# Kernel tuning notes

Hardware: AMD Instinct MI355X
Metric: run time of the kernel (lower is better)

Reference implementation:

```python
import jax, jax.numpy as jnp
import numpy as np

T, B, DIM, N = 2, 256, 512, 196


def setup_inputs() -> dict:
    key = jax.random.key(0)
    ks = jax.random.split(key, 6)
    scale_mem = (2.0 / (DIM + DIM)) ** 0.5      # GlorotNormal
    scale_cat = (2.0 / (2 * DIM + DIM)) ** 0.5
    scale_attn = (2.0 / (DIM + 1)) ** 0.5
    return {
        "memory": jax.random.normal(ks[0], (T, B, DIM), dtype=jnp.float32),
        "know": jax.random.normal(ks[1], (B, DIM, N), dtype=jnp.float32),
        "control": jax.random.normal(ks[2], (T, B, DIM), dtype=jnp.float32),
        "W_mem": jax.random.normal(ks[3], (DIM, DIM), dtype=jnp.float32) * scale_mem,
        "b_mem": jnp.zeros((DIM,), dtype=jnp.float32),
        "W_concat": jax.random.normal(ks[4], (2 * DIM, DIM), dtype=jnp.float32) * scale_cat,
        "b_concat": jnp.zeros((DIM,), dtype=jnp.float32),
        "W_attn": jax.random.normal(ks[5], (DIM, 1), dtype=jnp.float32) * scale_attn,
        "b_attn": jnp.zeros((1,), dtype=jnp.float32),
    }


def reference(memory, know, control, W_mem, b_mem, W_concat, b_concat, W_attn, b_attn):
    # mem = Dense(dim)(memory[-1]) -> [B, dim]
    mem = memory[-1] @ W_mem + b_mem
    # mem[..., None] * know -> [B, dim, N]; concat along channel axis -> [B, 2*dim, N]
    cat = jnp.concatenate([mem[:, :, None] * know, know], axis=1)
    # transpose to [B, N, 2*dim], Dense(dim) -> [B, N, dim]
    concat = jnp.swapaxes(cat, 1, 2) @ W_concat + b_concat
    # gate by control[-1] -> [B, N, dim]; Dense(1) + squeeze -> [B, N]
    attn = concat * control[-1][:, None, :]
    logits = jnp.squeeze(attn @ W_attn, -1) + b_attn[0]
    # softmax over N, then (faithfully) weighted sum over the dim axis -> [B, N]
    a = jax.nn.softmax(logits, axis=1)[:, None, :]  # [B, 1, N]
    read = jnp.sum(a * know, axis=1)  # [B, N]
    return read
```

## Files before the change

kernel.cpp:

```cpp
#include <hip/hip_runtime.h>
#include <cfloat>

#define BB   256
#define DIM  512
#define NN   196

typedef __attribute__((ext_vector_type(8))) short bf16x8;
typedef __attribute__((ext_vector_type(4))) float f32x4;

__device__ __forceinline__ ushort f2bf(float x) {
    unsigned u = __float_as_uint(x);
    return (ushort)((u + 0x7FFFu + ((u >> 16) & 1u)) >> 16);
}

__global__ __launch_bounds__(256) void convert_kernel(
    const float* __restrict__ memory, const float* __restrict__ control,
    const float* __restrict__ W_mem, const float* __restrict__ W_concat,
    const float* __restrict__ W_attn,
    ushort* __restrict__ Wt,
    ushort* __restrict__ mu)
{
    const int tid = threadIdx.x;
    const int blk = blockIdx.x;

    if (blk < 128) {
        const float4* in4 = (const float4*)W_concat;
        uint2* out = (uint2*)(Wt + (size_t)DIM * DIM);
        #pragma unroll
        for (int p = 0; p < 4; ++p) {
            const int idx = blk * 1024 + p * 256 + tid;
            const float4 q = in4[idx];
            uint2 o;
            o.x = (unsigned)f2bf(q.x) | ((unsigned)f2bf(q.y) << 16);
            o.y = (unsigned)f2bf(q.z) | ((unsigned)f2bf(q.w) << 16);
            out[idx] = o;
        }
    } else if (blk < 192) {
        __shared__ float T[64][65];
        const int t  = blk - 128;
        const int tk = (t >> 3) * 64, ti = (t & 7) * 64;
        const int r  = tid >> 2;
        const int cb = (tid & 3) * 16;
        #pragma unroll
        for (int j = 0; j < 16; j += 4) {
            const float4 q = *(const float4*)&W_mem[(size_t)(tk + r) * DIM + ti + cb + j];
            T[r][cb + j + 0] = q.x; T[r][cb + j + 1] = q.y;
            T[r][cb + j + 2] = q.z; T[r][cb + j + 3] = q.w;
        }
        __syncthreads();
        const int ii = tid & 63;
        const int kq = tid >> 6;
        #pragma unroll
        for (int kk = 0; kk < 16; kk += 2) {
            const int k = kq * 16 + kk;
            const unsigned v = (unsigned)f2bf(T[k][ii]) | ((unsigned)f2bf(T[k + 1][ii]) << 16);
            *(unsigned*)&Wt[(size_t)(ti + ii) * DIM + tk + k] = v;
        }
    } else {
        const float4* mem4 = (const float4*)(memory  + (size_t)BB * DIM);
        const float4* ctl4 = (const float4*)(control + (size_t)BB * DIM);
        const float4* wa4  = (const float4*)W_attn;
        uint2* out = (uint2*)mu;
        #pragma unroll
        for (int p = 0; p < 4; ++p) {
            const int idx = (blk - 192) * 1024 + p * 256 + tid;
            const int sec = idx >> 15;
            const int j   = idx & 32767;
            float4 q = sec ? ctl4[j] : mem4[j];
            if (sec) {
                const float4 wa = wa4[j & 127];
                q.x *= wa.x; q.y *= wa.y; q.z *= wa.z; q.w *= wa.w;
            }
            uint2 o;
            o.x = (unsigned)f2bf(q.x) | ((unsigned)f2bf(q.y) << 16);
            o.y = (unsigned)f2bf(q.z) | ((unsigned)f2bf(q.w) << 16);
            out[(size_t)sec * 32768 + j] = o;
        }
    }
}

__global__ __launch_bounds__(128) void prep_mfma(
    const ushort* __restrict__ Wt,
    const ushort* __restrict__ mu,
    const float* __restrict__ b_mem,
    float* __restrict__ w_out)
{
    __shared__ __align__(16) ushort mus[2][16][520];

    const int tid = threadIdx.x;
    const int wv  = tid >> 6;
    const int l   = tid & 63;
    const int b0  = blockIdx.x * 16;
    const int i0  = blockIdx.y * 32;

    #pragma unroll
    for (int p = 0; p < 16; ++p) {
        const int idx = p * 128 + tid;
        const int a   = idx >> 10;
        const int rb  = (idx >> 6) & 15;
        const int kc  = (idx & 63) * 8;
        *(uint4*)&mus[a][rb][kc] =
            *(const uint4*)&mu[((size_t)a * BB + b0 + rb) * DIM + kc];
    }
    __syncthreads();

    const int fr = l & 15;
    const int fk = (l >> 4) * 8;

    f32x4 accM = {0.f, 0.f, 0.f, 0.f};
    f32x4 acc1 = {0.f, 0.f, 0.f, 0.f};
    f32x4 acc2 = {0.f, 0.f, 0.f, 0.f};

    const int ib = i0 + wv * 16 + fr;
    const ushort* wm = Wt + ((size_t)0 * DIM + ib) * DIM;
    const ushort* c1 = Wt + ((size_t)1 * DIM + ib) * DIM;
    const ushort* c2 = Wt + ((size_t)2 * DIM + ib) * DIM;

    #pragma unroll 4
    for (int t = 0; t < 16; ++t) {
        const int k = t * 32 + fk;
        const bf16x8 am = *(const bf16x8*)&mus[0][fr][k];
        const bf16x8 au = *(const bf16x8*)&mus[1][fr][k];
        const bf16x8 bm = *(const bf16x8*)&wm[k];
        const bf16x8 b1 = *(const bf16x8*)&c1[k];
        const bf16x8 b2 = *(const bf16x8*)&c2[k];
        accM = __builtin_amdgcn_mfma_f32_16x16x32_bf16(am, bm, accM, 0, 0, 0);
        acc1 = __builtin_amdgcn_mfma_f32_16x16x32_bf16(au, b1, acc1, 0, 0, 0);
        acc2 = __builtin_amdgcn_mfma_f32_16x16x32_bf16(au, b2, acc2, 0, 0, 0);
    }

    const float bmv = b_mem[ib];
    const int rb0 = (l >> 4) * 4;
    #pragma unroll
    for (int r = 0; r < 4; ++r) {
        w_out[(size_t)(b0 + rb0 + r) * DIM + ib] =
            (accM[r] + bmv) * acc1[r] + acc2[r];
    }
}

__global__ __launch_bounds__(512, 4) void prep_fallback(
    const float* __restrict__ memory, const float* __restrict__ control,
    const float* __restrict__ W_mem, const float* __restrict__ b_mem,
    const float* __restrict__ W_concat, const float* __restrict__ W_attn,
    float* __restrict__ w_out)
{
    __shared__ float4 MU4[4][DIM];
    __shared__ float  buf[12288];

    const int tid = threadIdx.x;
    const int il  = tid & 31;
    const int kg  = tid >> 5;
    const int b0  = blockIdx.x * 8;
    const int i0  = blockIdx.y * 32;

    const float* mem_in = memory  + (size_t)BB * DIM;
    const float* ctl_in = control + (size_t)BB * DIM;

    {
        const float wa = W_attn[tid];
        #pragma unroll
        for (int p = 0; p < 4; ++p) {
            MU4[p][tid] = make_float4(
                mem_in[(size_t)(b0 + 2 * p)     * DIM + tid],
                ctl_in[(size_t)(b0 + 2 * p)     * DIM + tid] * wa,
                mem_in[(size_t)(b0 + 2 * p + 1) * DIM + tid],
                ctl_in[(size_t)(b0 + 2 * p + 1) * DIM + tid] * wa);
        }
    }

    float am[8] = {}, a1[8] = {}, a2[8] = {};
    const int sr = tid >> 4;
    const int sc = tid & 15;
    float2* WT = (float2*)buf;

    float4 f1 = *(const float4*)&W_concat[(size_t)(i0 + sr) * DIM + sc * 4];
    float4 f2 = *(const float4*)&W_concat[(size_t)(DIM + i0 + sr) * DIM + sc * 4];
    float wmc[4], wmn[4];
    #pragma unroll
    for (int j = 0; j < 4; ++j)
        wmc[j] = W_mem[(size_t)(kg * 4 + j) * DIM + i0 + il];

    for (int kt = 0; kt < DIM; kt += 64) {
        __syncthreads();
        {
            const float* f1f = (const float*)&f1;
            const float* f2f = (const float*)&f2;
            #pragma unroll
            for (int j = 0; j < 4; ++j)
                WT[(sc * 4 + j) * 33 + sr] = make_float2(f1f[j], f2f[j]);
        }
        if (kt + 64 < DIM) {
            f1 = *(const float4*)&W_concat[(size_t)(i0 + sr) * DIM + kt + 64 + sc * 4];
            f2 = *(const float4*)&W_concat[(size_t)(DIM + i0 + sr) * DIM + kt + 64 + sc * 4];
        }
        __syncthreads();
        if (kt + 64 < DIM) {
            #pragma unroll
            for (int j = 0; j < 4; ++j)
                wmn[j] = W_mem[(size_t)(kt + 64 + kg * 4 + j) * DIM + i0 + il];
        }
        #pragma unroll
        for (int j = 0; j < 4; ++j) {
            const int kl = kg * 4 + j;
            const int k  = kt + kl;
            const float2 c = WT[kl * 33 + il];
            #pragma unroll
            for (int p = 0; p < 4; ++p) {
                const float4 muv = MU4[p][k];
                am[2*p]   = fmaf(muv.x, wmc[j], am[2*p]);
                a1[2*p]   = fmaf(muv.y, c.x,    a1[2*p]);
                a2[2*p]   = fmaf(muv.y, c.y,    a2[2*p]);
                am[2*p+1] = fmaf(muv.z, wmc[j], am[2*p+1]);
                a1[2*p+1] = fmaf(muv.w, c.x,    a1[2*p+1]);
                a2[2*p+1] = fmaf(muv.w, c.y,    a2[2*p+1]);
            }
        }
        #pragma unroll
        for (int j = 0; j < 4; ++j) wmc[j] = wmn[j];
    }

    __syncthreads();
    #pragma unroll
    for (int b = 0; b < 8; ++b) {
        const int row = (kg * 8 + b) * 32 + il;
        buf[row]        = am[b];
        buf[4096 + row] = a1[b];
        buf[8192 + row] = a2[b];
    }
    __syncthreads();
    if (tid < 256) {
        const int rb = tid >> 5, ri = tid & 31;
        float sm = 0.f, s1 = 0.f, s2 = 0.f;
        #pragma unroll
        for (int t = 0; t < 16; ++t) {
            const int row = (t * 8 + rb) * 32 + ri;
            sm += buf[row];
            s1 += buf[4096 + row];
            s2 += buf[8192 + row];
        }
        w_out[(size_t)(b0 + rb) * DIM + i0 + ri] =
            (sm + b_mem[i0 + ri]) * s1 + s2;
    }
}

__global__ __launch_bounds__(1024) void read_kernel(
    const float* __restrict__ know,
    const float* __restrict__ w,
    float* __restrict__ out)
{
    __shared__ float  w_s[DIM];
    __shared__ float4 part_lg[16][50];
    __shared__ float4 part_ks[16][50];
    __shared__ float  tmp[256];
    __shared__ float  bc[2];

    const int tx  = threadIdx.x;
    const int ty  = threadIdx.y;
    const int tid = ty * 64 + tx;
    const int b   = blockIdx.x;

    if (tid < DIM) w_s[tid] = w[(size_t)b * DIM + tid];
    __syncthreads();

    float4 lg = make_float4(0.f, 0.f, 0.f, 0.f);
    float4 ks = make_float4(0.f, 0.f, 0.f, 0.f);
    if (tx < 49) {
        const float4* kp = (const float4*)(know + (size_t)b * DIM * NN) + (size_t)(ty * 32) * 49 + tx;
        const float*  wp = w_s + ty * 32;
        #pragma unroll 8
        for (int dd = 0; dd < 32; ++dd) {
            const float4 kv = kp[(size_t)dd * 49];
            const float  wv = wp[dd];
            lg.x = fmaf(kv.x, wv, lg.x); lg.y = fmaf(kv.y, wv, lg.y);
            lg.z = fmaf(kv.z, wv, lg.z); lg.w = fmaf(kv.w, wv, lg.w);
            ks.x += kv.x; ks.y += kv.y; ks.z += kv.z; ks.w += kv.w;
        }
        part_lg[ty][tx] = lg;
        part_ks[ty][tx] = ks;
    }
    __syncthreads();

    float lgn = 0.f, ksn = 0.f;
    if (tid < NN) {
        const int ng = tid >> 2, j = tid & 3;
        #pragma unroll
        for (int t = 0; t < 16; ++t) {
            lgn += ((const float*)&part_lg[t][ng])[j];
            ksn += ((const float*)&part_ks[t][ng])[j];
        }
    }

    if (tid < 256) tmp[tid] = (tid < NN) ? lgn : -FLT_MAX;
    __syncthreads();
    if (tid < 64) {
        float m = fmaxf(fmaxf(tmp[tid], tmp[tid + 64]),
                        fmaxf(tmp[tid + 128], tmp[tid + 192]));
        #pragma unroll
        for (int o = 32; o; o >>= 1) m = fmaxf(m, __shfl_down(m, o));
        if (tid == 0) bc[0] = m;
    }
    __syncthreads();

    const float e = (tid < NN) ? __expf(lgn - bc[0]) : 0.f;
    if (tid < 256) tmp[tid] = e;
    __syncthreads();
    if (tid < 64) {
        float s = tmp[tid] + tmp[tid + 64] + tmp[tid + 128] + tmp[tid + 192];
        #pragma unroll
        for (int o = 32; o; o >>= 1) s += __shfl_down(s, o);
        if (tid == 0) bc[1] = s;
    }
    __syncthreads();

    if (tid < NN) out[(size_t)b * NN + tid] = e / bc[1] * ksn;
}

extern "C" void kernel_launch(void* const* d_in, const int* in_sizes, int n_in,
                              void* d_out, int out_size, void* d_ws, size_t ws_size,
                              hipStream_t stream) {
    const float* memory   = (const float*)d_in[0];
    const float* know     = (const float*)d_in[1];
    const float* control  = (const float*)d_in[2];
    const float* W_mem    = (const float*)d_in[3];
    const float* b_mem    = (const float*)d_in[4];
    const float* W_concat = (const float*)d_in[5];
    const float* W_attn   = (const float*)d_in[7];
    float* outp = (float*)d_out;

    const size_t W_BYTES  = (size_t)BB * DIM * sizeof(float);
    const size_t WT_BYTES = (size_t)3 * DIM * DIM * sizeof(ushort);
    const size_t MU_BYTES = (size_t)2 * BB * DIM * sizeof(ushort);

    float* w_ws = (float*)d_ws;

    if (ws_size >= W_BYTES + WT_BYTES + MU_BYTES) {
        ushort* Wt = (ushort*)((char*)d_ws + W_BYTES);
        ushort* mu = (ushort*)((char*)d_ws + W_BYTES + WT_BYTES);
        convert_kernel<<<dim3(256), dim3(256), 0, stream>>>(
            memory, control, W_mem, W_concat, W_attn, Wt, mu);
        prep_mfma<<<dim3(BB / 16, DIM / 32), dim3(128), 0, stream>>>(
            Wt, mu, b_mem, w_ws);
    } else {
        prep_fallback<<<dim3(BB / 8, DIM / 32), dim3(512), 0, stream>>>(
            memory, control, W_mem, b_mem, W_concat, W_attn, w_ws);
    }
    read_kernel<<<dim3(BB), dim3(64, 16), 0, stream>>>(know, w_ws, outp);
}
```

Before: 33.12 us.

## Split-K the MFMA prep GEMM with atomics and defer combine to read kernel

Result: slower. 36.97 us (+11.6%).

```diff
diff --git a/kernel.cpp b/kernel.cpp
--- a/kernel.cpp
+++ b/kernel.cpp
@@ -23,21 +23,16 @@
     const int tid = threadIdx.x;
     const int blk = blockIdx.x;
 
-    if (blk < 128) {
-        const float4* in4 = (const float4*)W_concat;
-        uint2* out = (uint2*)(Wt + (size_t)DIM * DIM);
-        #pragma unroll
-        for (int p = 0; p < 4; ++p) {
-            const int idx = blk * 1024 + p * 256 + tid;
-            const float4 q = in4[idx];
-            uint2 o;
-            o.x = (unsigned)f2bf(q.x) | ((unsigned)f2bf(q.y) << 16);
-            o.y = (unsigned)f2bf(q.z) | ((unsigned)f2bf(q.w) << 16);
-            out[idx] = o;
-        }
-    } else if (blk < 192) {
+    if (blk < 512) {
+        const int idx = blk * 256 + tid;
+        const float4 q = ((const float4*)W_concat)[idx];
+        uint2 o;
+        o.x = (unsigned)f2bf(q.x) | ((unsigned)f2bf(q.y) << 16);
+        o.y = (unsigned)f2bf(q.z) | ((unsigned)f2bf(q.w) << 16);
+        ((uint2*)(Wt + (size_t)DIM * DIM))[idx] = o;
+    } else if (blk < 576) {
         __shared__ float T[64][65];
-        const int t  = blk - 128;
+        const int t  = blk - 512;
         const int tk = (t >> 3) * 64, ti = (t & 7) * 64;
         const int r  = tid >> 2;
         const int cb = (tid & 3) * 16;
@@ -57,50 +52,45 @@
             *(unsigned*)&Wt[(size_t)(ti + ii) * DIM + tk + k] = v;
         }
     } else {
-        const float4* mem4 = (const float4*)(memory  + (size_t)BB * DIM);
-        const float4* ctl4 = (const float4*)(control + (size_t)BB * DIM);
-        const float4* wa4  = (const float4*)W_attn;
-        uint2* out = (uint2*)mu;
-        #pragma unroll
-        for (int p = 0; p < 4; ++p) {
-            const int idx = (blk - 192) * 1024 + p * 256 + tid;
-            const int sec = idx >> 15;
-            const int j   = idx & 32767;
-            float4 q = sec ? ctl4[j] : mem4[j];
-            if (sec) {
-                const float4 wa = wa4[j & 127];
-                q.x *= wa.x; q.y *= wa.y; q.z *= wa.z; q.w *= wa.w;
-            }
-            uint2 o;
-            o.x = (unsigned)f2bf(q.x) | ((unsigned)f2bf(q.y) << 16);
-            o.y = (unsigned)f2bf(q.z) | ((unsigned)f2bf(q.w) << 16);
-            out[(size_t)sec * 32768 + j] = o;
-        }
+        const int idx = (blk - 576) * 256 + tid;
+        const int sec = idx >> 15;
+        const int j   = idx & 32767;
+        const float4* src = sec ? (const float4*)(control + (size_t)BB * DIM)
+                                : (const float4*)(memory  + (size_t)BB * DIM);
+        float4 q = src[j];
+        if (sec) {
+            const float4 wa = ((const float4*)W_attn)[j & 127];
+            q.x *= wa.x; q.y *= wa.y; q.z *= wa.z; q.w *= wa.w;
+        }
+        uint2 o;
+        o.x = (unsigned)f2bf(q.x) | ((unsigned)f2bf(q.y) << 16);
+        o.y = (unsigned)f2bf(q.z) | ((unsigned)f2bf(q.w) << 16);
+        ((uint2*)mu)[(size_t)sec * 32768 + j] = o;
     }
 }
 
 __global__ __launch_bounds__(128) void prep_mfma(
     const ushort* __restrict__ Wt,
     const ushort* __restrict__ mu,
-    const float* __restrict__ b_mem,
-    float* __restrict__ w_out)
+    float* __restrict__ P)
 {
-    __shared__ __align__(16) ushort mus[2][16][520];
+    __shared__ __align__(16) ushort mus[2][16][264];
 
     const int tid = threadIdx.x;
     const int wv  = tid >> 6;
     const int l   = tid & 63;
     const int b0  = blockIdx.x * 16;
     const int i0  = blockIdx.y * 32;
+    const int k0  = blockIdx.z * 256;
 
     #pragma unroll
-    for (int p = 0; p < 16; ++p) {
+    for (int p = 0; p < 8; ++p) {
         const int idx = p * 128 + tid;
-        const int a   = idx >> 10;
-        const int rb  = (idx >> 6) & 15;
-        const int kc  = (idx & 63) * 8;
+        const int a   = idx >> 9;
+        const int rb  = (idx >> 5) & 15;
+        const int kc  = (idx & 31) * 8;
         *(uint4*)&mus[a][rb][kc] =
-            *(const uint4*)&mu[((size_t)a * BB + b0 + rb) * DIM + kc];
+            *(const uint4*)&mu[((size_t)a * BB + b0 + rb) * DIM + k0 + kc];
     }
     __syncthreads();
 
@@ -112,12 +102,12 @@
     f32x4 acc2 = {0.f, 0.f, 0.f, 0.f};
 
     const int ib = i0 + wv * 16 + fr;
-    const ushort* wm = Wt + ((size_t)0 * DIM + ib) * DIM;
-    const ushort* c1 = Wt + ((size_t)1 * DIM + ib) * DIM;
-    const ushort* c2 = Wt + ((size_t)2 * DIM + ib) * DIM;
+    const ushort* wm = Wt + ((size_t)0 * DIM + ib) * DIM + k0;
+    const ushort* c1 = Wt + ((size_t)1 * DIM + ib) * DIM + k0;
+    const ushort* c2 = Wt + ((size_t)2 * DIM + ib) * DIM + k0;
 
     #pragma unroll 4
-    for (int t = 0; t < 16; ++t) {
+    for (int t = 0; t < 8; ++t) {
         const int k = t * 32 + fk;
         const bf16x8 am = *(const bf16x8*)&mus[0][fr][k];
         const bf16x8 au = *(const bf16x8*)&mus[1][fr][k];
@@ -129,13 +119,91 @@
         acc2 = __builtin_amdgcn_mfma_f32_16x16x32_bf16(au, b2, acc2, 0, 0, 0);
     }
 
-    const float bmv = b_mem[ib];
     const int rb0 = (l >> 4) * 4;
     #pragma unroll
     for (int r = 0; r < 4; ++r) {
-        w_out[(size_t)(b0 + rb0 + r) * DIM + ib] =
-            (accM[r] + bmv) * acc1[r] + acc2[r];
-    }
+        const size_t row = (size_t)(b0 + rb0 + r) * DIM + ib;
+        atomicAdd(&P[row],                         accM[r]);
+        atomicAdd(&P[(size_t)BB * DIM + row],      acc1[r]);
+        atomicAdd(&P[(size_t)2 * BB * DIM + row],  acc2[r]);
+    }
+}
+
+__global__ __launch_bounds__(1024) void read_kernel_p(
+    const float* __restrict__ know,
+    const float* __restrict__ P,
+    const float* __restrict__ b_mem,
+    float* __restrict__ out)
+{
+    __shared__ float  w_s[DIM];
+    __shared__ float4 part_lg[16][50];
+    __shared__ float4 part_ks[16][50];
+    __shared__ float  tmp[256];
+    __shared__ float  bc[2];
+
+    const int tx  = threadIdx.x;
+    const int ty  = threadIdx.y;
+    const int tid = ty * 64 + tx;
+    const int b   = blockIdx.x;
+
+    if (tid < DIM) {
+        const size_t row = (size_t)b * DIM + tid;
+        w_s[tid] = (P[row] + b_mem[tid]) * P[(size_t)BB * DIM + row]
+                 + P[(size_t)2 * BB * DIM + row];
+    }
+    __syncthreads();
+
+    float4 lg = make_float4(0.f, 0.f, 0.f, 0.f);
+    float4 ks = make_float4(0.f, 0.f, 0.f, 0.f);
+    if (tx < 49) {
+        const float4* kp = (const float4*)(know + (size_t)b * DIM * NN) + (size_t)(ty * 32) * 49 + tx;
+        const float*  wp = w_s + ty * 32;
+        #pragma unroll 8
+        for (int dd = 0; dd < 32; ++dd) {
+            const float4 kv = kp[(size_t)dd * 49];
+            const float  wv = wp[dd];
+            lg.x = fmaf(kv.x, wv, lg.x); lg.y = fmaf(kv.y, wv, lg.y);
+            lg.z = fmaf(kv.z, wv, lg.z); lg.w = fmaf(kv.w, wv, lg.w);
+            ks.x += kv.x; ks.y += kv.y; ks.z += kv.z; ks.w += kv.w;
+        }
+        part_lg[ty][tx] = lg;
+        part_ks[ty][tx] = ks;
+    }
+    __syncthreads();
+
+    float lgn = 0.f, ksn = 0.f;
+    if (tid < NN) {
+        const int ng = tid >> 2, j = tid & 3;
+        #pragma unroll
+        for (int t = 0; t < 16; ++t) {
+            lgn += ((const float*)&part_lg[t][ng])[j];
+            ksn += ((const float*)&part_ks[t][ng])[j];
+        }
+    }
+
+    if (tid < 256) tmp[tid] = (tid < NN) ? lgn : -FLT_MAX;
+    __syncthreads();
+    if (tid < 64) {
+        float m = fmaxf(fmaxf(tmp[tid], tmp[tid + 64]),
+                        fmaxf(tmp[tid + 128], tmp[tid + 192]));
+        #pragma unroll
+        for (int o = 32; o; o >>= 1) m = fmaxf(m, __shfl_down(m, o));
+        if (tid == 0) bc[0] = m;
+    }
+    __syncthreads();
+
+    const float e = (tid < NN) ? __expf(lgn - bc[0]) : 0.f;
+    if (tid < 256) tmp[tid] = e;
+    __syncthreads();
+    if (tid < 64) {
+        float s = tmp[tid] + tmp[tid + 64] + tmp[tid + 128] + tmp[tid + 192];
+        #pragma unroll
+        for (int o = 32; o; o >>= 1) s += __shfl_down(s, o);
+        if (tid == 0) bc[1] = s;
+    }
+    __syncthreads();
+
+    if (tid < NN) out[(size_t)b * NN + tid] = e / bc[1] * ksn;
 }
 
 __global__ __launch_bounds__(512, 4) void prep_fallback(
@@ -243,9 +311,8 @@
     }
 }
 
-__global__ __launch_bounds__(1024) void read_kernel(
-    const float* __restrict__ know,
-    const float* __restrict__ w,
+__global__ __launch_bounds__(1024) void read_kernel_w(
+    const float* __restrict__ know, const float* __restrict__ w,
     float* __restrict__ out)
 {
     __shared__ float  w_s[DIM];
@@ -327,22 +394,25 @@
     const float* W_attn   = (const float*)d_in[7];
     float* outp = (float*)d_out;
 
-    const size_t W_BYTES  = (size_t)BB * DIM * sizeof(float);
+    const size_t P_BYTES  = (size_t)3 * BB * DIM * sizeof(float);
     const size_t WT_BYTES = (size_t)3 * DIM * DIM * sizeof(ushort);
     const size_t MU_BYTES = (size_t)2 * BB * DIM * sizeof(ushort);
 
-    float* w_ws = (float*)d_ws;
-
-    if (ws_size >= W_BYTES + WT_BYTES + MU_BYTES) {
-        ushort* Wt = (ushort*)((char*)d_ws + W_BYTES);
-        ushort* mu = (ushort*)((char*)d_ws + W_BYTES + WT_BYTES);
-        convert_kernel<<<dim3(256), dim3(256), 0, stream>>>(
+    if (ws_size >= P_BYTES + WT_BYTES + MU_BYTES) {
+        float*  Pp = (float*)d_ws;
+        ushort* Wt = (ushort*)((char*)d_ws + P_BYTES);
+        ushort* mu = (ushort*)((char*)d_ws + P_BYTES + WT_BYTES);
+        hipMemsetAsync(Pp, 0, P_BYTES, stream);
+        convert_kernel<<<dim3(832), dim3(256), 0, stream>>>(
             memory, control, W_mem, W_concat, W_attn, Wt, mu);
-        prep_mfma<<<dim3(BB / 16, DIM / 32), dim3(128), 0, stream>>>(
-            Wt, mu, b_mem, w_ws);
+        prep_mfma<<<dim3(BB / 16, DIM / 32, 2), dim3(128), 0, stream>>>(
+            Wt, mu, Pp);
+        read_kernel_p<<<dim3(BB), dim3(64, 16), 0, stream>>>(
+            know, Pp, b_mem, outp);
     } else {
+        float* w_ws = (float*)d_ws;
         prep_fallback<<<dim3(BB / 8, DIM / 32), dim3(512), 0, stream>>>(
             memory, control, W_mem, b_mem, W_concat, W_attn, w_ws);
-    }
-    read_kernel<<<dim3(BB), dim3(64, 16), 0, stream>>>(know, w_ws, outp);
-}
+        read_kernel_w<<<dim3(BB), dim3(64, 16), 0, stream>>>(know, w_ws, outp);
+    }
+}
```
